# Optimization experiments

Measured on AMD Instinct MI355X. Metric: run time of the kernel, lower is better.

The kernel has to match this reference:

```python
import jax, jax.numpy as jnp
import numpy as np

T, B, F = 256, 256, 128   # seq_len, batch (graph nodes), feature_dim = graph_arch[0]
H1 = 256                  # graph_arch[1]
H = 128                   # graph_arch[-1] == lstm hidden_dim
Q = 4                     # n_qubits bottleneck per gate
TAGS = 32


def setup_inputs() -> dict:
    key = jax.random.key(0)
    ks = jax.random.split(key, 8)
    s = 0.05  # init scale for stability
    return {
        "node_sequences": jax.random.normal(ks[0], (T, B, F), jnp.float32),
        "adj": jax.random.uniform(ks[1], (B, B), jnp.float32),
        "W1": jax.random.normal(ks[2], (F, H1), jnp.float32) * s,
        "b1": jnp.zeros((H1,), jnp.float32),
        "W2": jax.random.normal(ks[3], (H1, H), jnp.float32) * s,
        "b2": jnp.zeros((H,), jnp.float32),
        "Win": jax.random.normal(ks[4], (4, F + H, Q), jnp.float32) * s,   # 4 gates: f,i,g,o
        "b_in": jnp.zeros((4, Q), jnp.float32),
        "Wout": jax.random.normal(ks[5], (4, Q, H), jnp.float32) * s,
        "b_out": jnp.zeros((4, H), jnp.float32),
        "Wtag": jax.random.normal(ks[6], (H, TAGS), jnp.float32) * s,
        "btag": jnp.zeros((TAGS,), jnp.float32),
    }


def reference(node_sequences, adj, W1, b1, W2, b2, Win, b_in, Wout, b_out, Wtag, btag):
    t, b, f = node_sequences.shape
    # per-node feedforward MLP (batched instead of the original per-sample loop)
    flat = node_sequences.reshape(t * b, f)
    a1 = jnp.tanh(flat @ W1 + b1)
    node_states = jnp.tanh(a1 @ W2 + b2).reshape(t, b, -1)   # [T,B,H]
    # fidelity-adjacency aggregation over the node (batch) axis
    aggregated = jnp.einsum('ij,tjf->tif', adj, node_states)  # [T,B,H]

    h_dim = Wout.shape[-1]

    def step(carry, x_t):
        h, c = carry
        v = jnp.concatenate([x_t, h], axis=-1)                       # [B, F+H]
        z = jnp.tanh(jnp.einsum('bv,gvq->gbq', v, Win) + b_in[:, None, :])   # quantum-layer bottleneck [4,B,Q]
        g = jnp.einsum('gbq,gqh->gbh', z, Wout) + b_out[:, None, :]          # [4,B,H]
        f_g = jax.nn.sigmoid(g[0])
        i_g = jax.nn.sigmoid(g[1])
        g_g = jnp.tanh(g[2])
        o_g = jax.nn.sigmoid(g[3])
        c = f_g * c + i_g * g_g
        h = o_g * jnp.tanh(c)
        return (h, c), h

    h0 = jnp.zeros((b, h_dim), node_sequences.dtype)
    c0 = jnp.zeros((b, h_dim), node_sequences.dtype)
    _, lstm_out = jax.lax.scan(step, (h0, c0), aggregated)   # [T,B,H]

    logits = lstm_out @ Wtag + btag                          # [T,B,TAGS]
    return jax.nn.log_softmax(logits, axis=2)
```

## Files before the change

kernel.cpp:

```cpp
#include <hip/hip_runtime.h>
#include <hip/hip_bf16.h>

#define T_DIM 256
#define B_DIM 256
#define F_DIM 128
#define H1_DIM 256
#define H_DIM 128
#define Q_DIM 4
#define TAGS 32
#define TB (T_DIM * B_DIM)

typedef __attribute__((ext_vector_type(8))) short bf16x8;
typedef __attribute__((ext_vector_type(4))) float f32x4;
typedef __attribute__((ext_vector_type(2))) float f32x2;

__device__ __forceinline__ float rcpf(float x) { return __builtin_amdgcn_rcpf(x); }
__device__ __forceinline__ float exp2f_hw(float x) { return __builtin_amdgcn_exp2f(x); }

__device__ __forceinline__ float tanhf_fast(float x) {
    float e = exp2f_hw(2.885390081777927f * x);
    return 1.0f - 2.0f * rcpf(e + 1.0f);
}
__device__ __forceinline__ float sigf(float x) {
    return rcpf(1.0f + exp2f_hw(-1.4426950408889634f * x));
}

__device__ __forceinline__ unsigned short f2bf(float f) {
    __hip_bfloat16 h = __float2bfloat16(f);
    return *reinterpret_cast<unsigned short*>(&h);
}

__device__ __forceinline__ f32x2 pk_mul2(f32x2 a, f32x2 b) {
    f32x2 d;
    asm("v_pk_mul_f32 %0, %1, %2" : "=v"(d) : "v"(a), "v"(b));
    return d;
}
__device__ __forceinline__ f32x2 pk_add2(f32x2 a, f32x2 b) {
    f32x2 d;
    asm("v_pk_add_f32 %0, %1, %2" : "=v"(d) : "v"(a), "v"(b));
    return d;
}
__device__ __forceinline__ f32x2 pk_fma2(f32x2 a, f32x2 b, f32x2 c) {
    f32x2 d;
    asm("v_pk_fma_f32 %0, %1, %2, %3" : "=v"(d) : "v"(a), "v"(b), "v"(c));
    return d;
}

template<int CTRL>
__device__ __forceinline__ float dpp_xadd(float x) {
    int t = __builtin_amdgcn_update_dpp(0, __float_as_int(x), CTRL, 0xF, 0xF, true);
    return x + __int_as_float(t);
}

__global__ __launch_bounds__(256) void prep_transpose_kernel(
    const float* __restrict__ W1, const float* __restrict__ W2,
    const float* __restrict__ Win, const float* __restrict__ Wtag,
    const float* __restrict__ adj,
    unsigned short* __restrict__ W1p, unsigned short* __restrict__ W2p,
    unsigned short* __restrict__ Winxp, unsigned short* __restrict__ Wtagp,
    float* __restrict__ adjT)
{
    __shared__ float tile[32][33];
    const int tid = threadIdx.x;
    if (blockIdx.x >= 64) {
        const int blk = blockIdx.x - 64;
        const int bx = blk & 7, by = blk >> 3;
        const int lx = tid & 31, ly = (tid >> 5) * 4;
#pragma unroll
        for (int r = 0; r < 4; r++)
            tile[ly + r][lx] = adj[(long)(by * 32 + ly + r) * 256 + bx * 32 + lx];
        __syncthreads();
#pragma unroll
        for (int r = 0; r < 4; r++)
            adjT[(long)(bx * 32 + ly + r) * 256 + by * 32 + lx] = tile[lx][ly + r];
        return;
    }
    const int gid0 = blockIdx.x * 256 + tid;
    const int gstride = 64 * 256;
    for (int idx = gid0; idx < 32768; idx += gstride) {
        int e = idx & 7, l = (idx >> 3) & 63, t2 = idx >> 9;
        int nb = t2 & 15, kk = t2 >> 4;
        int k = kk * 32 + (l >> 4) * 8 + e, n = nb * 16 + (l & 15);
        W1p[idx] = f2bf(W1[k * 256 + n]);
    }
    for (int idx = gid0; idx < 32768; idx += gstride) {
        int e = idx & 7, l = (idx >> 3) & 63, t2 = idx >> 9;
        int nb = t2 & 7, kk = t2 >> 3;
        int k = kk * 32 + (l >> 4) * 8 + e, n = nb * 16 + (l & 15);
        W2p[idx] = f2bf(W2[k * 128 + n]);
    }
    for (int idx = gid0; idx < 2048; idx += gstride) {
        int e = idx & 7, l = (idx >> 3) & 63, kk = idx >> 9;
        int k = kk * 32 + (l >> 4) * 8 + e, o = l & 15;
        Winxp[idx] = f2bf(Win[(o >> 2) * 1024 + k * 4 + (o & 3)]);
    }
    for (int idx = gid0; idx < 4096; idx += gstride) {
        int e = idx & 7, l = (idx >> 3) & 63, t2 = idx >> 9;
        int nt = t2 & 1, kk = t2 >> 1;
        int k = kk * 32 + (l >> 4) * 8 + e, n = nt * 16 + (l & 15);
        Wtagp[idx] = f2bf(Wtag[k * 32 + n]);
    }
}

__global__ __launch_bounds__(256) void mlp_mfma_kernel(
    const float* __restrict__ X, const unsigned short* __restrict__ W1p,
    const float* __restrict__ b1, const unsigned short* __restrict__ W2p,
    const float* __restrict__ b2, const unsigned short* __restrict__ Winxp,
    float* __restrict__ NSP)
{
    __shared__ __align__(16) unsigned short a1_s[64 * 256];
    __shared__ __align__(16) unsigned short xns_s[64 * 128];

    const int tid = threadIdx.x;
    const int w = tid >> 6;
    const int lane = tid & 63;
    const int lr = lane & 15;
    const int lg = lane >> 4;
    const long rowbase = (long)blockIdx.x * 64;

    char* const a1c = (char*)a1_s;
    char* const xnc = (char*)xns_s;

    {
        const int r = tid >> 2;
        const int qc = tid & 3;
        const float4* xg = (const float4*)(X + (rowbase + r) * 128 + qc * 32);
#pragma unroll
        for (int i = 0; i < 4; i++) {
            float4 lo = xg[i * 2], hi = xg[i * 2 + 1];
            bf16x8 v;
            v[0] = (short)f2bf(lo.x); v[1] = (short)f2bf(lo.y);
            v[2] = (short)f2bf(lo.z); v[3] = (short)f2bf(lo.w);
            v[4] = (short)f2bf(hi.x); v[5] = (short)f2bf(hi.y);
            v[6] = (short)f2bf(hi.z); v[7] = (short)f2bf(hi.w);
            int byte = (r * 256 + qc * 64 + i * 16) ^ ((r & 7) << 4);
            *(bf16x8*)(xnc + byte) = v;
        }
    }
    __syncthreads();

    {
        f32x4 acc[4][4];
#pragma unroll
        for (int mi = 0; mi < 4; mi++)
#pragma unroll
            for (int j = 0; j < 4; j++) acc[mi][j] = (f32x4){0.f, 0.f, 0.f, 0.f};

        const bf16x8* w1v = (const bf16x8*)W1p;
#pragma unroll
        for (int kk = 0; kk < 4; kk++) {
            bf16x8 af[4];
#pragma unroll
            for (int mi = 0; mi < 4; mi++) {
                int row = mi * 16 + lr;
                int byte = (row * 256 + kk * 64 + lg * 16) ^ ((row & 7) << 4);
                af[mi] = *(const bf16x8*)(xnc + byte);
            }
            bf16x8 bfv[4];
#pragma unroll
            for (int j = 0; j < 4; j++)
                bfv[j] = w1v[(kk * 16 + (w * 4 + j)) * 64 + lane];
#pragma unroll
            for (int mi = 0; mi < 4; mi++)
#pragma unroll
                for (int j = 0; j < 4; j++)
                    acc[mi][j] = __builtin_amdgcn_mfma_f32_16x16x32_bf16(
                        af[mi], bfv[j], acc[mi][j], 0, 0, 0);
        }

        float b1v[4];
#pragma unroll
        for (int j = 0; j < 4; j++) b1v[j] = b1[(w * 4 + j) * 16 + lr];
#pragma unroll
        for (int mi = 0; mi < 4; mi++)
#pragma unroll
            for (int j = 0; j < 4; j++)
#pragma unroll
                for (int reg = 0; reg < 4; reg++) {
                    int row = mi * 16 + lg * 4 + reg;
                    int col = (w * 4 + j) * 16 + lr;
                    float v = tanhf_fast(acc[mi][j][reg] + b1v[j]);
                    int byte = (row * 512 + col * 2) ^ ((row & 7) << 4);
                    *(unsigned short*)(a1c + byte) = f2bf(v);
                }
    }
    __syncthreads();

    {
        f32x4 acc[4][2];
#pragma unroll
        for (int mi = 0; mi < 4; mi++)
#pragma unroll
            for (int j = 0; j < 2; j++) acc[mi][j] = (f32x4){0.f, 0.f, 0.f, 0.f};

        const bf16x8* w2v = (const bf16x8*)W2p;
#pragma unroll
        for (int kk = 0; kk < 8; kk++) {
            bf16x8 af[4];
#pragma unroll
            for (int mi = 0; mi < 4; mi++) {
                int row = mi * 16 + lr;
                int byte = (row * 512 + kk * 64 + lg * 16) ^ ((row & 7) << 4);
                af[mi] = *(const bf16x8*)(a1c + byte);
            }
            bf16x8 bfv[2];
#pragma unroll
            for (int j = 0; j < 2; j++)
                bfv[j] = w2v[(kk * 8 + (w * 2 + j)) * 64 + lane];
#pragma unroll
            for (int mi = 0; mi < 4; mi++)
#pragma unroll
                for (int j = 0; j < 2; j++)
                    acc[mi][j] = __builtin_amdgcn_mfma_f32_16x16x32_bf16(
                        af[mi], bfv[j], acc[mi][j], 0, 0, 0);
        }

        float b2v[2];
#pragma unroll
        for (int j = 0; j < 2; j++) b2v[j] = b2[(w * 2 + j) * 16 + lr];
#pragma unroll
        for (int mi = 0; mi < 4; mi++)
#pragma unroll
            for (int j = 0; j < 2; j++)
#pragma unroll
                for (int reg = 0; reg < 4; reg++) {
                    int row = mi * 16 + lg * 4 + reg;
                    int col = (w * 2 + j) * 16 + lr;
                    float v = tanhf_fast(acc[mi][j][reg] + b2v[j]);
                    int byte = (row * 256 + col * 2) ^ ((row & 7) << 4);
                    *(unsigned short*)(xnc + byte) = f2bf(v);
                }
    }
    __syncthreads();

    {
        f32x4 acc = (f32x4){0.f, 0.f, 0.f, 0.f};
        const bf16x8* wxv = (const bf16x8*)Winxp;
#pragma unroll
        for (int kk = 0; kk < 4; kk++) {
            int row = w * 16 + lr;
            int byte = (row * 256 + kk * 64 + lg * 16) ^ ((row & 7) << 4);
            bf16x8 af = *(const bf16x8*)(xnc + byte);
            bf16x8 bfv = wxv[kk * 64 + lane];
            acc = __builtin_amdgcn_mfma_f32_16x16x32_bf16(af, bfv, acc, 0, 0, 0);
        }
#pragma unroll
        for (int reg = 0; reg < 4; reg++) {
            int row = w * 16 + lg * 4 + reg;
            NSP[(rowbase + row) * 16 + lr] = acc[reg];
        }
    }
}

__global__ __launch_bounds__(256) void aggx_kernel(
    const float* __restrict__ adjT, const float* __restrict__ NSP,
    const float* __restrict__ b_in, float* __restrict__ AX)
{
    __shared__ float4 nsp_s[256 * 4];
    const int tid = threadIdx.x;
    const int t = blockIdx.x;
    {
        const float4* g = (const float4*)(NSP + (long)t * 4096);
#pragma unroll
        for (int i = 0; i < 4; i++) nsp_s[tid + i * 256] = g[tid + i * 256];
    }
    __syncthreads();

    float4 acc[4];
#pragma unroll
    for (int p = 0; p < 4; p++) acc[p] = ((const float4*)b_in)[p];

    const float* arow = adjT + tid;
    float a[8], an[8];
#pragma unroll
    for (int m = 0; m < 8; m++) an[m] = arow[m * 256];
    for (int j0 = 0; j0 < 256; j0 += 8) {
#pragma unroll
        for (int m = 0; m < 8; m++) a[m] = an[m];
        if (j0 + 8 < 256) {
#pragma unroll
            for (int m = 0; m < 8; m++) an[m] = arow[(j0 + 8 + m) * 256];
        }
#pragma unroll
        for (int m = 0; m < 8; m++) {
            float av = a[m];
#pragma unroll
            for (int p = 0; p < 4; p++) {
                float4 nv = nsp_s[(j0 + m) * 4 + p];
                acc[p].x += av * nv.x; acc[p].y += av * nv.y;
                acc[p].z += av * nv.z; acc[p].w += av * nv.w;
            }
        }
    }
    float4* out = (float4*)(AX + (long)t * 4096 + tid * 16);
#pragma unroll
    for (int p = 0; p < 4; p++) out[p] = acc[p];
}

__device__ __forceinline__ int hhoff(int row, int inrow) {
    return (row * 512 + inrow) ^ ((row & 7) << 4);
}

__global__ __attribute__((amdgpu_waves_per_eu(1, 1))) __launch_bounds__(128)
void lstm_head_kernel(
    const float* __restrict__ AX, const float* __restrict__ Win,
    const float* __restrict__ Wout, const float* __restrict__ b_out,
    const unsigned short* __restrict__ Wtagp, const float* __restrict__ btag,
    float* __restrict__ OUT)
{
    __shared__ __align__(16) float hh[T_DIM * 128];
    char* const hhc = (char*)hh;

    const int tid = threadIdx.x;
    const int w = tid >> 6;
    const int lane = tid & 63;
    const int b = blockIdx.x;
    const int o = lane >> 2;
    const int s = lane & 3;
    const int g_o = o >> 2, q_o = o & 3;

    f32x2 wh2[16];
#pragma unroll
    for (int m = 0; m < 8; m++)
#pragma unroll
        for (int p = 0; p < 2; p++) {
            int k0 = m * 16 + s * 4 + p * 2;
            f32x2 v;
            v.x = Win[g_o * 1024 + 512 + k0 * 4 + q_o];
            v.y = Win[g_o * 1024 + 512 + (k0 + 1) * 4 + q_o];
            wh2[m * 2 + p] = v;
        }
    {
        const bool sw = (w == 1);
#pragma unroll
        for (int i = 0; i < 8; i++) {
            f32x2 a = wh2[i], bv = wh2[i + 8];
            wh2[i]     = sw ? bv : a;
            wh2[i + 8] = sw ? a : bv;
        }
    }

    const int f = w * 64 + lane;
    float wo[4][4];
    float bo[4];
#pragma unroll
    for (int g = 0; g < 4; g++) {
        bo[g] = b_out[g * 128 + f];
#pragma unroll
        for (int q = 0; q < 4; q++)
            wo[g][q] = Wout[(g * 4 + q) * 128 + f];
    }

    const int own_off = w << 8;
    const int oth_off = own_off ^ 256;
    int woffs[8], roffs[8];
#pragma unroll
    for (int sl = 0; sl < 8; sl++) {
        woffs[sl] = ((lane * 4) ^ (sl << 4)) + own_off;
        roffs[sl] = (s * 16) ^ ((sl << 4) & 0x30);
    }

    float c = 0.f;
    f32x2 hown[8], hoth[8];
#pragma unroll
    for (int m = 0; m < 8; m++) { hown[m] = (f32x2){0.f, 0.f}; hoth[m] = (f32x2){0.f, 0.f}; }

    const float* axp = AX + (long)b * 16 + o;
    float ax_cur = axp[0];
    float ax_nxt = axp[B_DIM * 16];
    axp += 2 * B_DIM * 16;

    int vbase = 0;
    for (int tb = 0; tb < T_DIM; tb += 8) {
#pragma unroll
        for (int sl = 0; sl < 8; sl++) {
            const int sw6 = (sl << 4) & 0x40;
            f32x2 aA = pk_mul2(hown[0], wh2[0]);
            f32x2 aB = pk_mul2(hown[1], wh2[1]);
            f32x2 aC = pk_mul2(hown[2], wh2[2]);
            f32x2 aD = pk_mul2(hown[3], wh2[3]);
            aA = pk_fma2(hown[4], wh2[4], aA);
            aB = pk_fma2(hown[5], wh2[5], aB);
            aC = pk_fma2(hown[6], wh2[6], aC);
            aD = pk_fma2(hown[7], wh2[7], aD);
            aA = pk_fma2(hoth[0], wh2[8],  aA);
            aB = pk_fma2(hoth[1], wh2[9],  aB);
            aC = pk_fma2(hoth[2], wh2[10], aC);
            aD = pk_fma2(hoth[3], wh2[11], aD);
            aA = pk_fma2(hoth[4], wh2[12], aA);
            aB = pk_fma2(hoth[5], wh2[13], aB);
            aC = pk_fma2(hoth[6], wh2[14], aC);
            aD = pk_fma2(hoth[7], wh2[15], aD);
            f32x2 sAB = pk_add2(aA, aB);
            f32x2 sCD = pk_add2(aC, aD);
            f32x2 sS  = pk_add2(sAB, sCD);
            float acc = sS.x + sS.y;
            acc = dpp_xadd<0xB1>(acc);
            acc = dpp_xadd<0x4E>(acc);
            float zv = tanhf_fast(acc + ax_cur);

            unsigned zb = __float_as_uint(zv);
            float z[16];
#pragma unroll
            for (int oo = 0; oo < 16; oo++)
                z[oo] = __uint_as_float(__builtin_amdgcn_readlane(zb, oo * 4));

            {
                float gp_f = bo[0] + z[0]*wo[0][0] + z[1]*wo[0][1] + z[2]*wo[0][2] + z[3]*wo[0][3];
                float gp_i = bo[1] + z[4]*wo[1][0] + z[5]*wo[1][1] + z[6]*wo[1][2] + z[7]*wo[1][3];
                float gp_g = bo[2] + z[8]*wo[2][0] + z[9]*wo[2][1] + z[10]*wo[2][2] + z[11]*wo[2][3];
                float gp_o = bo[3] + z[12]*wo[3][0] + z[13]*wo[3][1] + z[14]*wo[3][2] + z[15]*wo[3][3];
                float fg = sigf(gp_f);
                float ig = sigf(gp_i);
                float gg = tanhf_fast(gp_g);
                float og = sigf(gp_o);
                c = fg * c + ig * gg;
                float hval = og * tanhf_fast(c);
                *(float*)(hhc + vbase + sl * 512 + woffs[sl]) = hval;
            }

            const char* const rp = hhc + vbase + sl * 512 + roffs[sl];
#pragma unroll
            for (int m = 0; m < 4; m++) {
                float4 v4 = *(const float4*)(rp + own_off + ((m * 64) ^ sw6));
                hown[m * 2]     = (f32x2){v4.x, v4.y};
                hown[m * 2 + 1] = (f32x2){v4.z, v4.w};
            }

            __syncthreads();

            ax_cur = ax_nxt;
            ax_nxt = *axp;
            axp += B_DIM * 16;

#pragma unroll
            for (int m = 0; m < 4; m++) {
                float4 v4 = *(const float4*)(rp + oth_off + ((m * 64) ^ sw6));
                hoth[m * 2]     = (f32x2){v4.x, v4.y};
                hoth[m * 2 + 1] = (f32x2){v4.z, v4.w};
            }
        }
        vbase += 8 * 512;
    }

    const int lr = lane & 15;
    const int lg = lane >> 4;
    const bf16x8* wtv = (const bf16x8*)Wtagp;
    bf16x8 wt[4][2];
#pragma unroll
    for (int kk = 0; kk < 4; kk++)
#pragma unroll
        for (int nt = 0; nt < 2; nt++)
            wt[kk][nt] = wtv[(kk * 2 + nt) * 64 + lane];
    float bt0 = btag[lr], bt1 = btag[16 + lr];

    for (int mi = w * 8; mi < w * 8 + 8; mi++) {
        f32x4 acc0 = (f32x4){0.f, 0.f, 0.f, 0.f};
        f32x4 acc1 = (f32x4){0.f, 0.f, 0.f, 0.f};
        const int arow = mi * 16 + lr;
#pragma unroll
        for (int kk = 0; kk < 4; kk++) {
            float4 lo = *(const float4*)(hhc + hhoff(arow, kk * 128 + lg * 32));
            float4 hi = *(const float4*)(hhc + hhoff(arow, kk * 128 + lg * 32 + 16));
            bf16x8 af;
            af[0] = (short)f2bf(lo.x); af[1] = (short)f2bf(lo.y);
            af[2] = (short)f2bf(lo.z); af[3] = (short)f2bf(lo.w);
            af[4] = (short)f2bf(hi.x); af[5] = (short)f2bf(hi.y);
            af[6] = (short)f2bf(hi.z); af[7] = (short)f2bf(hi.w);
            acc0 = __builtin_amdgcn_mfma_f32_16x16x32_bf16(af, wt[kk][0], acc0, 0, 0, 0);
            acc1 = __builtin_amdgcn_mfma_f32_16x16x32_bf16(af, wt[kk][1], acc1, 0, 0, 0);
        }
        float s0[4], s1[4], mx[4], se[4];
#pragma unroll
        for (int reg = 0; reg < 4; reg++) {
            s0[reg] = acc0[reg] + bt0;
            s1[reg] = acc1[reg] + bt1;
            float m = fmaxf(s0[reg], s1[reg]);
#pragma unroll
            for (int d = 8; d >= 1; d >>= 1) m = fmaxf(m, __shfl_xor(m, d));
            mx[reg] = m;
            float e = __expf(s0[reg] - m) + __expf(s1[reg] - m);
#pragma unroll
            for (int d = 8; d >= 1; d >>= 1) e += __shfl_xor(e, d);
            se[reg] = __logf(e);
        }
#pragma unroll
        for (int reg = 0; reg < 4; reg++) {
            long t = mi * 16 + lg * 4 + reg;
            long base = (t * B_DIM + b) * 32;
            OUT[base + lr]      = s0[reg] - mx[reg] - se[reg];
            OUT[base + 16 + lr] = s1[reg] - mx[reg] - se[reg];
        }
    }
}

extern "C" void kernel_launch(void* const* d_in, const int* in_sizes, int n_in,
                              void* d_out, int out_size, void* d_ws, size_t ws_size,
                              hipStream_t stream)
{
    const float* X    = (const float*)d_in[0];
    const float* adj  = (const float*)d_in[1];
    const float* W1   = (const float*)d_in[2];
    const float* b1   = (const float*)d_in[3];
    const float* W2   = (const float*)d_in[4];
    const float* b2   = (const float*)d_in[5];
    const float* Win  = (const float*)d_in[6];
    const float* b_in = (const float*)d_in[7];
    const float* Wout = (const float*)d_in[8];
    const float* bout = (const float*)d_in[9];
    const float* Wtag = (const float*)d_in[10];
    const float* btag = (const float*)d_in[11];
    float* OUT = (float*)d_out;

    float* ws = (float*)d_ws;
    float* NSP  = ws;
    float* adjT = ws + 1048576;
    float* AX   = ws + 1114112;
    unsigned short* W1p   = (unsigned short*)(ws + 2162688);
    unsigned short* W2p   = W1p + 32768;
    unsigned short* Winxp = W2p + 32768;
    unsigned short* Wtagp = Winxp + 2048;

    prep_transpose_kernel<<<dim3(128), dim3(256), 0, stream>>>(
        W1, W2, Win, Wtag, adj, W1p, W2p, Winxp, Wtagp, adjT);
    mlp_mfma_kernel<<<dim3(TB / 64), dim3(256), 0, stream>>>(X, W1p, b1, W2p, b2, Winxp, NSP);
    aggx_kernel<<<dim3(256), dim3(256), 0, stream>>>(adjT, NSP, b_in, AX);
    lstm_head_kernel<<<dim3(B_DIM), dim3(128), 0, stream>>>(AX, Win, Wout, bout, Wtagp, btag, OUT);
}
```

Baseline: 136.8 us.

## Split recurrent h·Win reduction across waves, exchange partial sums via LDS

Each of the two waves now computes only its own half of the hidden-state dot product with Win, writes the partial sum to a double-buffered LDS scratch, syncs, and adds the other wave's partial before the tanh. Previously each wave read the full h vector (both halves) after the barrier. This halves per-step FMA and LDS read work on the serial critical path and drops the post-barrier read of the other half. The cost is an extra LDS write/read of partials and a barrier placed earlier in the step, plus one more barrier before the tag head.

```diff
diff --git a/kernel.cpp b/kernel.cpp
--- a/kernel.cpp
+++ b/kernel.cpp
@@ -309,6 +309,7 @@
     float* __restrict__ OUT)
 {
     __shared__ __align__(16) float hh[T_DIM * 128];
+    __shared__ __align__(16) float zbuf[2 * 128];
     char* const hhc = (char*)hh;
 
     const int tid = threadIdx.x;
@@ -319,26 +320,17 @@
     const int s = lane & 3;
     const int g_o = o >> 2, q_o = o & 3;
 
-    f32x2 wh2[16];
-#pragma unroll
-    for (int m = 0; m < 8; m++)
+    f32x2 wh2[8];
+#pragma unroll
+    for (int m = 0; m < 4; m++)
 #pragma unroll
         for (int p = 0; p < 2; p++) {
-            int k0 = m * 16 + s * 4 + p * 2;
+            int k0 = w * 64 + m * 16 + s * 4 + p * 2;
             f32x2 v;
             v.x = Win[g_o * 1024 + 512 + k0 * 4 + q_o];
             v.y = Win[g_o * 1024 + 512 + (k0 + 1) * 4 + q_o];
             wh2[m * 2 + p] = v;
         }
-    {
-        const bool sw = (w == 1);
-#pragma unroll
-        for (int i = 0; i < 8; i++) {
-            f32x2 a = wh2[i], bv = wh2[i + 8];
-            wh2[i]     = sw ? bv : a;
-            wh2[i + 8] = sw ? a : bv;
-        }
-    }
 
     const int f = w * 64 + lane;
     float wo[4][4];
@@ -352,18 +344,20 @@
     }
 
     const int own_off = w << 8;
-    const int oth_off = own_off ^ 256;
+    const float axmask = (w == 0) ? 1.0f : 0.0f;
+    const int zw_idx = (w << 6) + lane;
+    const int zr_idx = ((w ^ 1) << 6) + lane;
     int woffs[8], roffs[8];
 #pragma unroll
     for (int sl = 0; sl < 8; sl++) {
         woffs[sl] = ((lane * 4) ^ (sl << 4)) + own_off;
-        roffs[sl] = (s * 16) ^ ((sl << 4) & 0x30);
+        roffs[sl] = ((s * 16) ^ ((sl << 4) & 0x30)) + own_off;
     }
 
     float c = 0.f;
-    f32x2 hown[8], hoth[8];
-#pragma unroll
-    for (int m = 0; m < 8; m++) { hown[m] = (f32x2){0.f, 0.f}; hoth[m] = (f32x2){0.f, 0.f}; }
+    f32x2 hz[8];
+#pragma unroll
+    for (int m = 0; m < 8; m++) hz[m] = (f32x2){0.f, 0.f};
 
     const float* axp = AX + (long)b * 16 + o;
     float ax_cur = axp[0];
@@ -375,35 +369,36 @@
 #pragma unroll
         for (int sl = 0; sl < 8; sl++) {
             const int sw6 = (sl << 4) & 0x40;
-            f32x2 aA = pk_mul2(hown[0], wh2[0]);
-            f32x2 aB = pk_mul2(hown[1], wh2[1]);
-            f32x2 aC = pk_mul2(hown[2], wh2[2]);
-            f32x2 aD = pk_mul2(hown[3], wh2[3]);
-            aA = pk_fma2(hown[4], wh2[4], aA);
-            aB = pk_fma2(hown[5], wh2[5], aB);
-            aC = pk_fma2(hown[6], wh2[6], aC);
-            aD = pk_fma2(hown[7], wh2[7], aD);
-            aA = pk_fma2(hoth[0], wh2[8],  aA);
-            aB = pk_fma2(hoth[1], wh2[9],  aB);
-            aC = pk_fma2(hoth[2], wh2[10], aC);
-            aD = pk_fma2(hoth[3], wh2[11], aD);
-            aA = pk_fma2(hoth[4], wh2[12], aA);
-            aB = pk_fma2(hoth[5], wh2[13], aB);
-            aC = pk_fma2(hoth[6], wh2[14], aC);
-            aD = pk_fma2(hoth[7], wh2[15], aD);
-            f32x2 sAB = pk_add2(aA, aB);
-            f32x2 sCD = pk_add2(aC, aD);
-            f32x2 sS  = pk_add2(sAB, sCD);
-            float acc = sS.x + sS.y;
-            acc = dpp_xadd<0xB1>(acc);
-            acc = dpp_xadd<0x4E>(acc);
-            float zv = tanhf_fast(acc + ax_cur);
-
-            unsigned zb = __float_as_uint(zv);
+            f32x2 aA = pk_mul2(hz[0], wh2[0]);
+            f32x2 aB = pk_mul2(hz[1], wh2[1]);
+            aA = pk_fma2(hz[2], wh2[2], aA);
+            aB = pk_fma2(hz[3], wh2[3], aB);
+            aA = pk_fma2(hz[4], wh2[4], aA);
+            aB = pk_fma2(hz[5], wh2[5], aB);
+            aA = pk_fma2(hz[6], wh2[6], aA);
+            aB = pk_fma2(hz[7], wh2[7], aB);
+            f32x2 sS = pk_add2(aA, aB);
+            float part = sS.x + sS.y;
+            part = dpp_xadd<0xB1>(part);
+            part = dpp_xadd<0x4E>(part);
+            part = fmaf(axmask, ax_cur, part);
+
+            float* zb = zbuf + ((sl & 1) << 7);
+            zb[zw_idx] = part;
+
+            __syncthreads();
+
+            ax_cur = ax_nxt;
+            ax_nxt = *axp;
+            axp += B_DIM * 16;
+
+            float zv = tanhf_fast(part + zb[zr_idx]);
+
+            unsigned zb32 = __float_as_uint(zv);
             float z[16];
 #pragma unroll
             for (int oo = 0; oo < 16; oo++)
-                z[oo] = __uint_as_float(__builtin_amdgcn_readlane(zb, oo * 4));
+                z[oo] = __uint_as_float(__builtin_amdgcn_readlane(zb32, oo * 4));
 
             {
                 float gp_f = bo[0] + z[0]*wo[0][0] + z[1]*wo[0][1] + z[2]*wo[0][2] + z[3]*wo[0][3];
@@ -422,22 +417,8 @@
             const char* const rp = hhc + vbase + sl * 512 + roffs[sl];
 #pragma unroll
             for (int m = 0; m < 4; m++) {
-                float4 v4 = *(const float4*)(rp + own_off + ((m * 64) ^ sw6));
-                hown[m * 2]     = (f32x2){v4.x, v4.y};
-                hown[m * 2 + 1] = (f32x2){v4.z, v4.w};
-            }
-
-            __syncthreads();
-
-            ax_cur = ax_nxt;
-            ax_nxt = *axp;
-            axp += B_DIM * 16;
-
-#pragma unroll
-            for (int m = 0; m < 4; m++) {
-                float4 v4 = *(const float4*)(rp + oth_off + ((m * 64) ^ sw6));
-                hoth[m * 2]     = (f32x2){v4.x, v4.y};
-                hoth[m * 2 + 1] = (f32x2){v4.z, v4.w};
+                hz[m * 2]     = *(const f32x2*)(rp + ((m * 64) ^ sw6));
+                hz[m * 2 + 1] = *(const f32x2*)(rp + ((m * 64) ^ sw6) + 8);
             }
         }
         vbase += 8 * 512;
@@ -453,6 +434,8 @@
         for (int nt = 0; nt < 2; nt++)
             wt[kk][nt] = wtv[(kk * 2 + nt) * 64 + lane];
     float bt0 = btag[lr], bt1 = btag[16 + lr];
+
+    __syncthreads();
 
     for (int mi = w * 8; mi < w * 8 + 8; mi++) {
         f32x4 acc0 = (f32x4){0.f, 0.f, 0.f, 0.f};
```

Result: slower. 141.0 us (+3.1%).
